# Kernel optimization log

Measured on AMD Instinct MI355X. Metric: run time of the kernel, lower is better.

## Reference

```python
import jax, jax.numpy as jnp
import numpy as np

N_EMBD = 1024
HEAD_SIZE = 64  # n_embd // n_head = 1024 // 16


def setup_inputs() -> dict:
    key = jax.random.key(0)
    ks = jax.random.split(key, 7)
    s = 0.02
    return {
        "x": jax.random.normal(ks[0], (8, 2048, N_EMBD), dtype=jnp.float32),
        "wq": jax.random.normal(ks[1], (N_EMBD, HEAD_SIZE), dtype=jnp.float32) * s,
        "bq": jax.random.normal(ks[2], (HEAD_SIZE,), dtype=jnp.float32) * s,
        "wk": jax.random.normal(ks[3], (N_EMBD, HEAD_SIZE), dtype=jnp.float32) * s,
        "bk": jax.random.normal(ks[4], (HEAD_SIZE,), dtype=jnp.float32) * s,
        "wv": jax.random.normal(ks[5], (N_EMBD, HEAD_SIZE), dtype=jnp.float32) * s,
        "bv": jax.random.normal(ks[6], (HEAD_SIZE,), dtype=jnp.float32) * s,
    }


def reference(x, wq, bq, wk, bk, wv, bv):
    B, T, C = x.shape
    q = x @ wq + bq  # [B,T,H]
    k = x @ wk + bk
    v = x @ wv + bv
    # NOTE: original scales by C**-0.5 where C = n_embd (full embedding dim)
    scale = jnp.asarray(C, x.dtype) ** -0.5
    att = jnp.einsum("bqh,bkh->bqk", q, k) * scale  # [B,T,T]
    causal = jnp.tril(jnp.ones((T, T), dtype=bool))
    att = jnp.where(causal, att, -jnp.inf)
    att = jax.nn.softmax(att, axis=-1)
    return jnp.einsum("bqk,bkh->bqh", att, v)  # [B,T,H]
```

## Files before the change

### kernel.cpp

```cpp
#include <hip/hip_runtime.h>
#include <hip/hip_bf16.h>

typedef short s8v __attribute__((ext_vector_type(8)));
typedef short s4v __attribute__((ext_vector_type(4)));
typedef float f4v __attribute__((ext_vector_type(4)));

#define MFMA16(a,b,c) __builtin_amdgcn_mfma_f32_16x16x32_bf16((a),(b),(c),0,0,0)

__device__ __forceinline__ short f2bf(float f) {
    __hip_bfloat16 h = __float2bfloat16(f);
    short s; __builtin_memcpy(&s, &h, 2); return s;
}
__device__ __forceinline__ float bf2f(short s) {
    unsigned int u = ((unsigned int)(unsigned short)s) << 16;
    float f; __builtin_memcpy(&f, &u, 4); return f;
}
__device__ __forceinline__ s4v cvt4(float4 a) {
    s4v r; r[0] = f2bf(a.x); r[1] = f2bf(a.y); r[2] = f2bf(a.z); r[3] = f2bf(a.w);
    return r;
}
__device__ __forceinline__ unsigned int pk2(float a, float b) {
    return ((unsigned int)(unsigned short)f2bf(b) << 16) |
           (unsigned int)(unsigned short)f2bf(a);
}

__global__ __launch_bounds__(256) void pack_w_kernel(
    const float* __restrict__ wq, const float* __restrict__ wk,
    const float* __restrict__ wv, short* __restrict__ wpack)
{
    int fid  = blockIdx.x * 256 + threadIdx.x;
    int lane = fid & 63;
    int ks   = (fid >> 6) & 31;
    int t    = fid >> 11;
    int m3 = t >> 2, nt = t & 3;
    int col = nt * 16 + (lane & 15);
    int k0  = ks * 32 + (lane >> 4) * 8;
    const float* w = (m3 == 0) ? wq : (m3 == 1 ? wk : wv);
    float sc = (m3 == 0) ? 0.03125f : 1.0f;
    s8v frag;
#pragma unroll
    for (int j = 0; j < 8; j++) frag[j] = f2bf(w[(k0 + j) * 64 + col] * sc);
    ((s8v*)wpack)[fid] = frag;
}

__global__ __launch_bounds__(256) void qkv_kernel(
    const float* __restrict__ x, const short* __restrict__ wpack,
    const float* __restrict__ bq, const float* __restrict__ bk,
    const float* __restrict__ bv,
    short* __restrict__ qws, short* __restrict__ kws, short* __restrict__ vt)
{
    __shared__ short xl[2][32][136];

    int tid  = threadIdx.x;
    int wave = tid >> 6, lane = tid & 63;
    int quad = lane >> 4, l16 = lane & 15;
    int row0 = blockIdx.x * 32;
    const float* xbase = x + (size_t)row0 * 1024;
    const s8v* wp = (const s8v*)wpack;
    int tbase = wave * 3;

    f4v acc[2][3];
    f4v z = {0.f, 0.f, 0.f, 0.f};
#pragma unroll
    for (int rf = 0; rf < 2; rf++)
#pragma unroll
        for (int i = 0; i < 3; i++) acc[rf][i] = z;

    float4 xr[4];
#pragma unroll
    for (int i = 0; i < 4; i++) {
        int idx = i * 256 + tid;
        xr[i] = *(const float4*)(xbase + (size_t)(idx >> 5) * 1024 + (idx & 31) * 4);
    }
#pragma unroll
    for (int i = 0; i < 4; i++) {
        int idx = i * 256 + tid;
        *(s4v*)&xl[0][idx >> 5][(idx & 31) * 4] = cvt4(xr[i]);
    }
    __syncthreads();

    for (int sk = 0; sk < 8; sk++) {
        int cur = sk & 1, nxt = cur ^ 1;
        if (sk < 7) {
#pragma unroll
            for (int i = 0; i < 4; i++) {
                int idx = i * 256 + tid;
                xr[i] = *(const float4*)(xbase + (size_t)(idx >> 5) * 1024
                                         + (sk + 1) * 128 + (idx & 31) * 4);
            }
        }
#pragma unroll
        for (int ks = 0; ks < 4; ks++) {
            s8v a0 = *(const s8v*)&xl[cur][l16][ks * 32 + quad * 8];
            s8v a1 = *(const s8v*)&xl[cur][16 + l16][ks * 32 + quad * 8];
            int kg = sk * 4 + ks;
#pragma unroll
            for (int i = 0; i < 3; i++) {
                s8v bf = wp[((tbase + i) * 32 + kg) * 64 + lane];
                acc[0][i] = MFMA16(a0, bf, acc[0][i]);
                acc[1][i] = MFMA16(a1, bf, acc[1][i]);
            }
        }
        if (sk < 7) {
#pragma unroll
            for (int i = 0; i < 4; i++) {
                int idx = i * 256 + tid;
                *(s4v*)&xl[nxt][idx >> 5][(idx & 31) * 4] = cvt4(xr[i]);
            }
        }
        __syncthreads();
    }

    int b = row0 >> 11;
#pragma unroll
    for (int rf = 0; rf < 2; rf++) {
        int rowD = row0 + rf * 16 + quad * 4;
#pragma unroll
        for (int i = 0; i < 3; i++) {
            int t = tbase + i, m3 = t >> 2, nt = t & 3;
            int col = nt * 16 + l16;
            if (m3 == 0) {
                float bias = bq[col] * 0.03125f;
#pragma unroll
                for (int r = 0; r < 4; r++)
                    qws[(rowD + r) * 64 + col] = f2bf(acc[rf][i][r] + bias);
            } else if (m3 == 1) {
                float bias = bk[col];
#pragma unroll
                for (int r = 0; r < 4; r++)
                    kws[(rowD + r) * 64 + col] = f2bf(acc[rf][i][r] + bias);
            } else {
                float bias = bv[col];
                int keyb = rowD & 2047;
                s4v v4;
#pragma unroll
                for (int r = 0; r < 4; r++) v4[r] = f2bf(acc[rf][i][r] + bias);
                *(s4v*)(vt + (size_t)(b * 64 + col) * 2048 + keyb) = v4;
            }
        }
    }
}

__global__ __launch_bounds__(256) void attn_kernel(
    const short* __restrict__ qws, const short* __restrict__ kws,
    const short* __restrict__ vt, short* __restrict__ opart,
    float* __restrict__ lpart)
{
    __shared__ short Kl[64][72];
    __shared__ short Vl[64][72];
    __shared__ short Pl[4][16 * 72];

    int tid  = threadIdx.x;
    int wave = tid >> 6, lane = tid & 63;
    int quad = lane >> 4, l16 = lane & 15;
    int b = blockIdx.y;
    int u = 143 - blockIdx.x;

    int g = 0;
#pragma unroll
    for (int gg = 1; gg <= 7; gg++) if (u >= 2 * gg * (gg + 1)) g = gg;
    int rem = u - 2 * g * (g + 1);
    int qt = 4 * g + rem / (g + 1);
    int cc = rem % (g + 1);

    int q0 = qt * 64;
    int c0 = cc * 256;
    bool last = (cc == g);
    int jtN = last ? (((q0 + 63 - c0) >> 6) + 1) : 4;

    const short* qb  = qws + (size_t)b * 2048 * 64;
    const short* kb  = kws + (size_t)b * 2048 * 64;
    const short* vtb = vt  + (size_t)b * 64 * 2048;

    int qrow = q0 + wave * 16 + l16;
    s8v qf0 = *(const s8v*)(qb + qrow * 64 + quad * 8);
    s8v qf1 = *(const s8v*)(qb + qrow * 64 + 32 + quad * 8);

    s8v onef;
#pragma unroll
    for (int j = 0; j < 8; j++) onef[j] = (l16 == 0) ? (short)0x3F80 : (short)0;

    f4v o[5];
    f4v z = {0.f, 0.f, 0.f, 0.f};
#pragma unroll
    for (int nt = 0; nt < 5; nt++) o[nt] = z;

    int srow = tid >> 3;
    int sc   = (tid & 7) * 8;

    s8v kr[2], vr[2];
#pragma unroll
    for (int i = 0; i < 2; i++) {
        int r = srow + i * 32;
        kr[i] = *(const s8v*)(kb + (c0 + r) * 64 + sc);
        vr[i] = *(const s8v*)(vtb + (size_t)r * 2048 + c0 + sc);
    }

    for (int t = 0; t < jtN; t++) {
        int key0 = c0 + t * 64;
        bool more = (t + 1 < jtN);

        __syncthreads();
#pragma unroll
        for (int i = 0; i < 2; i++) {
            int r = srow + i * 32;
            *(s8v*)&Kl[r][sc] = kr[i];
            *(s8v*)&Vl[r][sc] = vr[i];
        }
        __syncthreads();

        if (more) {
            int key1 = key0 + 64;
#pragma unroll
            for (int i = 0; i < 2; i++) {
                int r = srow + i * 32;
                kr[i] = *(const s8v*)(kb + (key1 + r) * 64 + sc);
                vr[i] = *(const s8v*)(vtb + (size_t)r * 2048 + key1 + sc);
            }
        }

        f4v s[4];
#pragma unroll
        for (int nt = 0; nt < 4; nt++) {
            s8v k0 = *(const s8v*)&Kl[nt * 16 + l16][quad * 8];
            s8v k1 = *(const s8v*)&Kl[nt * 16 + l16][32 + quad * 8];
            s[nt] = MFMA16(k0, qf0, z);
            s[nt] = MFMA16(k1, qf1, s[nt]);
        }

        if (last) {
            int qg = q0 + wave * 16 + l16;
#pragma unroll
            for (int nt = 0; nt < 4; nt++) {
                int keyb = key0 + nt * 16 + quad * 4;
#pragma unroll
                for (int r = 0; r < 4; r++)
                    if (keyb + r > qg) s[nt][r] = -1e30f;
            }
        }

        short* pw = Pl[wave];
#pragma unroll
        for (int nt = 0; nt < 4; nt++) {
            uint2 d;
            d.x = pk2(__expf(s[nt][0]), __expf(s[nt][1]));
            d.y = pk2(__expf(s[nt][2]), __expf(s[nt][3]));
            *(uint2*)&pw[l16 * 72 + nt * 16 + quad * 4] = d;
        }
        asm volatile("s_waitcnt lgkmcnt(0)" ::: "memory");

#pragma unroll
        for (int st = 0; st < 2; st++) {
            s8v pf = *(const s8v*)(pw + l16 * 72 + st * 32 + quad * 8);
#pragma unroll
            for (int nt = 0; nt < 4; nt++) {
                s8v vf = *(const s8v*)&Vl[nt * 16 + l16][st * 32 + quad * 8];
                o[nt] = MFMA16(pf, vf, o[nt]);
            }
            o[4] = MFMA16(pf, onef, o[4]);
        }
    }

    int g0 = b * 2048 + q0 + wave * 16;
    short* op = opart + (size_t)cc * (16384 * 64);
#pragma unroll
    for (int nt = 0; nt < 4; nt++)
#pragma unroll
        for (int r = 0; r < 4; r++)
            op[(size_t)(g0 + quad * 4 + r) * 64 + nt * 16 + l16] = f2bf(o[nt][r]);
    if (l16 == 0) {
        float* lp = lpart + (size_t)cc * 16384;
#pragma unroll
        for (int r = 0; r < 4; r++) lp[g0 + quad * 4 + r] = o[4][r];
    }
}

__global__ __launch_bounds__(256) void combine_kernel(
    const short* __restrict__ opart, const float* __restrict__ lpart,
    float* __restrict__ out)
{
    int idx = blockIdx.x * 256 + threadIdx.x;
    int g = idx >> 4;
    int d = (idx & 15) * 4;
    int nc = ((g & 2047) >> 8) + 1;
    float s0 = 0.f, s1 = 0.f, s2 = 0.f, s3 = 0.f, lsum = 0.f;
    for (int c = 0; c < nc; c++) {
        short4 o4 = *(const short4*)(opart + (size_t)c * (16384 * 64) + g * 64 + d);
        s0 += bf2f(o4.x); s1 += bf2f(o4.y); s2 += bf2f(o4.z); s3 += bf2f(o4.w);
        lsum += lpart[c * 16384 + g];
    }
    float inv = 1.0f / lsum;
    float4 res = {s0 * inv, s1 * inv, s2 * inv, s3 * inv};
    *(float4*)(out + g * 64 + d) = res;
}

extern "C" void kernel_launch(void* const* d_in, const int* in_sizes, int n_in,
                              void* d_out, int out_size, void* d_ws, size_t ws_size,
                              hipStream_t stream) {
    const float* x  = (const float*)d_in[0];
    const float* wq = (const float*)d_in[1];
    const float* bq = (const float*)d_in[2];
    const float* wk = (const float*)d_in[3];
    const float* bk = (const float*)d_in[4];
    const float* wv = (const float*)d_in[5];
    const float* bv = (const float*)d_in[6];
    float* out = (float*)d_out;

    char* ws = (char*)d_ws;
    short* wpack = (short*)ws;
    short* qws   = (short*)(ws + (512u << 10));
    short* kws   = (short*)(ws + (512u << 10) + (2u << 20));
    short* vt    = (short*)(ws + (512u << 10) + (4u << 20));
    short* opart = (short*)(ws + (512u << 10) + (6u << 20));
    float* lpart = (float*)(ws + (512u << 10) + (22u << 20));

    hipLaunchKernelGGL(pack_w_kernel,  dim3(96),        dim3(256), 0, stream,
                       wq, wk, wv, wpack);
    hipLaunchKernelGGL(qkv_kernel,     dim3(512),       dim3(256), 0, stream,
                       x, wpack, bq, bk, bv, qws, kws, vt);
    hipLaunchKernelGGL(attn_kernel,    dim3(144, 8),    dim3(256), 0, stream,
                       qws, kws, vt, opart, lpart);
    hipLaunchKernelGGL(combine_kernel, dim3(1024),      dim3(256), 0, stream,
                       opart, lpart, out);
}
```

Baseline: 134.8 us.

## Enlarge attention query tile to 128 rows with 8-wave blocks

Each attention block now covers 128 query rows using 8 waves (512 threads) instead of 64 rows with 4 waves. The block-to-(query tile, key chunk) mapping is rewritten for the triangular causal schedule, and each thread stages one K/V row slice instead of two. The aim is to share each loaded K/V tile across twice as many queries, cutting global and LDS traffic per query. In exchange the grid has half as many blocks, so load balance is coarser and the diagonal tiles carry more masked work.

```diff
diff --git a/kernel.cpp b/kernel.cpp
--- a/kernel.cpp
+++ b/kernel.cpp
@@ -141,32 +141,37 @@
     }
 }
 
-__global__ __launch_bounds__(256) void attn_kernel(
+__global__ __launch_bounds__(512) void attn_kernel(
     const short* __restrict__ qws, const short* __restrict__ kws,
     const short* __restrict__ vt, short* __restrict__ opart,
     float* __restrict__ lpart)
 {
     __shared__ short Kl[64][72];
     __shared__ short Vl[64][72];
-    __shared__ short Pl[4][16 * 72];
+    __shared__ short Pl[8][16 * 72];
 
     int tid  = threadIdx.x;
     int wave = tid >> 6, lane = tid & 63;
     int quad = lane >> 4, l16 = lane & 15;
     int b = blockIdx.y;
-    int u = 143 - blockIdx.x;
-
-    int g = 0;
-#pragma unroll
-    for (int gg = 1; gg <= 7; gg++) if (u >= 2 * gg * (gg + 1)) g = gg;
-    int rem = u - 2 * g * (g + 1);
-    int qt = 4 * g + rem / (g + 1);
-    int cc = rem % (g + 1);
-
-    int q0 = qt * 64;
+    int u = 71 - blockIdx.x;
+
+    int qt = 0;
+#pragma unroll
+    for (int q = 1; q < 16; q++) {
+        int m = q >> 1;
+        int st = (q & 1) ? (m + 1) * (m + 1) : m * (m + 1);
+        if (u >= st) qt = q;
+    }
+    int mq = qt >> 1;
+    int stq = (qt & 1) ? (mq + 1) * (mq + 1) : mq * (mq + 1);
+    int cc  = u - stq;
+    int nch = mq + 1;
+
+    int q0 = qt * 128;
     int c0 = cc * 256;
-    bool last = (cc == g);
-    int jtN = last ? (((q0 + 63 - c0) >> 6) + 1) : 4;
+    bool last = (cc == nch - 1);
+    int jtN = last ? (((q0 + 127 - c0) >> 6) + 1) : 4;
 
     const short* qb  = qws + (size_t)b * 2048 * 64;
     const short* kb  = kws + (size_t)b * 2048 * 64;
@@ -186,37 +191,25 @@
     for (int nt = 0; nt < 5; nt++) o[nt] = z;
 
     int srow = tid >> 3;
-    int sc   = (tid & 7) * 8;
-
-    s8v kr[2], vr[2];
-#pragma unroll
-    for (int i = 0; i < 2; i++) {
-        int r = srow + i * 32;
-        kr[i] = *(const s8v*)(kb + (c0 + r) * 64 + sc);
-        vr[i] = *(const s8v*)(vtb + (size_t)r * 2048 + c0 + sc);
-    }
+    int sc   = (tid & 3) * 16 + (tid & 4) * 2;
+    sc = (tid & 7) * 8;
+
+    s8v kr = *(const s8v*)(kb + (c0 + srow) * 64 + sc);
+    s8v vr = *(const s8v*)(vtb + (size_t)srow * 2048 + c0 + sc);
 
     for (int t = 0; t < jtN; t++) {
         int key0 = c0 + t * 64;
         bool more = (t + 1 < jtN);
 
         __syncthreads();
-#pragma unroll
-        for (int i = 0; i < 2; i++) {
-            int r = srow + i * 32;
-            *(s8v*)&Kl[r][sc] = kr[i];
-            *(s8v*)&Vl[r][sc] = vr[i];
-        }
+        *(s8v*)&Kl[srow][sc] = kr;
+        *(s8v*)&Vl[srow][sc] = vr;
         __syncthreads();
 
         if (more) {
             int key1 = key0 + 64;
-#pragma unroll
-            for (int i = 0; i < 2; i++) {
-                int r = srow + i * 32;
-                kr[i] = *(const s8v*)(kb + (key1 + r) * 64 + sc);
-                vr[i] = *(const s8v*)(vtb + (size_t)r * 2048 + key1 + sc);
-            }
+            kr = *(const s8v*)(kb + (key1 + srow) * 64 + sc);
+            vr = *(const s8v*)(vtb + (size_t)srow * 2048 + key1 + sc);
         }
 
         f4v s[4];
@@ -318,7 +311,7 @@
                        wq, wk, wv, wpack);
     hipLaunchKernelGGL(qkv_kernel,     dim3(512),       dim3(256), 0, stream,
                        x, wpack, bq, bk, bv, qws, kws, vt);
-    hipLaunchKernelGGL(attn_kernel,    dim3(144, 8),    dim3(256), 0, stream,
+    hipLaunchKernelGGL(attn_kernel,    dim3(72, 8),     dim3(512), 0, stream,
                        qws, kws, vt, opart, lpart);
     hipLaunchKernelGGL(combine_kernel, dim3(1024),      dim3(256), 0, stream,
                        opart, lpart, out);
```

After: 137.4 us. Within noise of the previous version (+1.9%).

## Store Q/K/V in MFMA fragment order and load attention operands directly from global

Applied to the files above, without the earlier changes.

The QKV projection now writes Q, K and V in a pre-swizzled layout that matches the MFMA operand fragments. The attention kernel can then load each lane's K and V fragments directly from global memory (L2), with no LDS staging and no block-wide barriers. The grid is flattened to 1D with the batch in the low bits, so blocks sharing the same K/V tile run close together. The trade-off is that each wave now reads K/V separately and relies on cache hits instead of shared memory, and it drops the explicit prefetch double-buffering.

```diff
diff --git a/kernel.cpp b/kernel.cpp
--- a/kernel.cpp
+++ b/kernel.cpp
@@ -23,6 +23,7 @@
     return ((unsigned int)(unsigned short)f2bf(b) << 16) |
            (unsigned int)(unsigned short)f2bf(a);
 }
+
 
 __global__ __launch_bounds__(256) void pack_w_kernel(
     const float* __restrict__ wq, const float* __restrict__ wk,
@@ -111,7 +112,6 @@
         __syncthreads();
     }
 
-    int b = row0 >> 11;
 #pragma unroll
     for (int rf = 0; rf < 2; rf++) {
         int rowD = row0 + rf * 16 + quad * 4;
@@ -122,39 +122,50 @@
             if (m3 == 0) {
                 float bias = bq[col] * 0.03125f;
 #pragma unroll
-                for (int r = 0; r < 4; r++)
-                    qws[(rowD + r) * 64 + col] = f2bf(acc[rf][i][r] + bias);
+                for (int r = 0; r < 4; r++) {
+                    int row = rowD + r;
+                    size_t a = (size_t)(row >> 4) * 1024 + (size_t)(col >> 5) * 512
+                             + (size_t)((col >> 3) & 3) * 128 + (row & 15) * 8 + (col & 7);
+                    qws[a] = f2bf(acc[rf][i][r] + bias);
+                }
             } else if (m3 == 1) {
                 float bias = bk[col];
 #pragma unroll
-                for (int r = 0; r < 4; r++)
-                    kws[(rowD + r) * 64 + col] = f2bf(acc[rf][i][r] + bias);
+                for (int r = 0; r < 4; r++) {
+                    int key = rowD + r;
+                    size_t a = (size_t)(key >> 6) * 4096
+                             + (size_t)((((key >> 4) & 3) * 2) + (col >> 5)) * 512
+                             + (size_t)((col >> 3) & 3) * 128 + (key & 15) * 8 + (col & 7);
+                    kws[a] = f2bf(acc[rf][i][r] + bias);
+                }
             } else {
                 float bias = bv[col];
-                int keyb = rowD & 2047;
+                int key = rowD;
+                size_t a = (size_t)(key >> 6) * 4096
+                         + (size_t)((col >> 4) * 2 + ((key >> 5) & 1)) * 512
+                         + (size_t)((key >> 3) & 3) * 128 + (col & 15) * 8 + (key & 7);
                 s4v v4;
 #pragma unroll
                 for (int r = 0; r < 4; r++) v4[r] = f2bf(acc[rf][i][r] + bias);
-                *(s4v*)(vt + (size_t)(b * 64 + col) * 2048 + keyb) = v4;
+                *(s4v*)(vt + a) = v4;
             }
         }
     }
 }
 
 __global__ __launch_bounds__(256) void attn_kernel(
-    const short* __restrict__ qws, const short* __restrict__ kws,
-    const short* __restrict__ vt, short* __restrict__ opart,
+    const short* __restrict__ qfa, const short* __restrict__ kfa,
+    const short* __restrict__ vfa, short* __restrict__ opart,
     float* __restrict__ lpart)
 {
-    __shared__ short Kl[64][72];
-    __shared__ short Vl[64][72];
     __shared__ short Pl[4][16 * 72];
 
     int tid  = threadIdx.x;
     int wave = tid >> 6, lane = tid & 63;
     int quad = lane >> 4, l16 = lane & 15;
-    int b = blockIdx.y;
-    int u = 143 - blockIdx.x;
+    int bid  = blockIdx.x;
+    int b    = bid & 7;
+    int u    = 143 - (bid >> 3);
 
     int g = 0;
 #pragma unroll
@@ -168,13 +179,10 @@
     bool last = (cc == g);
     int jtN = last ? (((q0 + 63 - c0) >> 6) + 1) : 4;
 
-    const short* qb  = qws + (size_t)b * 2048 * 64;
-    const short* kb  = kws + (size_t)b * 2048 * 64;
-    const short* vtb = vt  + (size_t)b * 64 * 2048;
-
-    int qrow = q0 + wave * 16 + l16;
-    s8v qf0 = *(const s8v*)(qb + qrow * 64 + quad * 8);
-    s8v qf1 = *(const s8v*)(qb + qrow * 64 + 32 + quad * 8);
+    const short* qbase = qfa + (size_t)((b * 2048 + q0 + wave * 16) >> 4) * 1024
+                       + lane * 8;
+    s8v qf0 = *(const s8v*)(qbase);
+    s8v qf1 = *(const s8v*)(qbase + 512);
 
     s8v onef;
 #pragma unroll
@@ -185,49 +193,29 @@
 #pragma unroll
     for (int nt = 0; nt < 5; nt++) o[nt] = z;
 
-    int srow = tid >> 3;
-    int sc   = (tid & 7) * 8;
-
-    s8v kr[2], vr[2];
-#pragma unroll
-    for (int i = 0; i < 2; i++) {
-        int r = srow + i * 32;
-        kr[i] = *(const s8v*)(kb + (c0 + r) * 64 + sc);
-        vr[i] = *(const s8v*)(vtb + (size_t)r * 2048 + c0 + sc);
-    }
+    short* pw = Pl[wave];
 
     for (int t = 0; t < jtN; t++) {
         int key0 = c0 + t * 64;
-        bool more = (t + 1 < jtN);
-
-        __syncthreads();
-#pragma unroll
-        for (int i = 0; i < 2; i++) {
-            int r = srow + i * 32;
-            *(s8v*)&Kl[r][sc] = kr[i];
-            *(s8v*)&Vl[r][sc] = vr[i];
-        }
-        __syncthreads();
-
-        if (more) {
-            int key1 = key0 + 64;
-#pragma unroll
-            for (int i = 0; i < 2; i++) {
-                int r = srow + i * 32;
-                kr[i] = *(const s8v*)(kb + (key1 + r) * 64 + sc);
-                vr[i] = *(const s8v*)(vtb + (size_t)r * 2048 + key1 + sc);
-            }
-        }
+        const short* kb_ = kfa + (size_t)(b * 32 + (key0 >> 6)) * 4096 + lane * 8;
+        const short* vb_ = vfa + (size_t)(b * 32 + (key0 >> 6)) * 4096 + lane * 8;
 
         f4v s[4];
 #pragma unroll
         for (int nt = 0; nt < 4; nt++) {
-            s8v k0 = *(const s8v*)&Kl[nt * 16 + l16][quad * 8];
-            s8v k1 = *(const s8v*)&Kl[nt * 16 + l16][32 + quad * 8];
+            s8v k0 = *(const s8v*)(kb_ + (nt * 2 + 0) * 512);
+            s8v k1 = *(const s8v*)(kb_ + (nt * 2 + 1) * 512);
             s[nt] = MFMA16(k0, qf0, z);
             s[nt] = MFMA16(k1, qf1, s[nt]);
         }
 
+        s8v vfr[8];
+#pragma unroll
+        for (int st = 0; st < 2; st++)
+#pragma unroll
+            for (int nt = 0; nt < 4; nt++)
+                vfr[st * 4 + nt] = *(const s8v*)(vb_ + (nt * 2 + st) * 512);
+
         if (last) {
             int qg = q0 + wave * 16 + l16;
 #pragma unroll
@@ -239,7 +227,6 @@
             }
         }
 
-        short* pw = Pl[wave];
 #pragma unroll
         for (int nt = 0; nt < 4; nt++) {
             uint2 d;
@@ -247,16 +234,13 @@
             d.y = pk2(__expf(s[nt][2]), __expf(s[nt][3]));
             *(uint2*)&pw[l16 * 72 + nt * 16 + quad * 4] = d;
         }
-        asm volatile("s_waitcnt lgkmcnt(0)" ::: "memory");
 
 #pragma unroll
         for (int st = 0; st < 2; st++) {
             s8v pf = *(const s8v*)(pw + l16 * 72 + st * 32 + quad * 8);
 #pragma unroll
-            for (int nt = 0; nt < 4; nt++) {
-                s8v vf = *(const s8v*)&Vl[nt * 16 + l16][st * 32 + quad * 8];
-                o[nt] = MFMA16(pf, vf, o[nt]);
-            }
+            for (int nt = 0; nt < 4; nt++)
+                o[nt] = MFMA16(pf, vfr[st * 4 + nt], o[nt]);
             o[4] = MFMA16(pf, onef, o[4]);
         }
     }
@@ -318,7 +302,7 @@
                        wq, wk, wv, wpack);
     hipLaunchKernelGGL(qkv_kernel,     dim3(512),       dim3(256), 0, stream,
                        x, wpack, bq, bk, bv, qws, kws, vt);
-    hipLaunchKernelGGL(attn_kernel,    dim3(144, 8),    dim3(256), 0, stream,
+    hipLaunchKernelGGL(attn_kernel,    dim3(1152),      dim3(256), 0, stream,
                        qws, kws, vt, opart, lpart);
     hipLaunchKernelGGL(combine_kernel, dim3(1024),      dim3(256), 0, stream,
                        opart, lpart, out);
```

Result: no change. 136.5 us (+1.3%).
